# Performance work log

Hardware: AMD Instinct MI355X
Metric: run time of the kernel (lower is better)

Reference implementation:

```python
import jax, jax.numpy as jnp
import numpy as np

N_SRC0, N_DST0, N_DST1 = 100000, 20000, 4000
E0, E1 = 640000, 128000
IN_F, HID_F, OUT_F = 512, 512, 256


def _graph_conv(x_src, src, dst, W, b, n_src, n_dst):
    """DGL GraphConv, norm='both': D_out^{-1/2} A D_in^{-1/2} X W + b."""
    ones_e = jnp.ones(src.shape[0], x_src.dtype)
    out_deg = jnp.maximum(jax.ops.segment_sum(ones_e, src, num_segments=n_src), 1.0)
    in_deg = jnp.maximum(jax.ops.segment_sum(ones_e, dst, num_segments=n_dst), 1.0)
    h = x_src * (out_deg ** -0.5)[:, None]          # [n_src, F] pre-normalize
    agg = jax.ops.segment_sum(h[src], dst, num_segments=n_dst)  # gather -> scatter-add
    agg = agg * (in_deg ** -0.5)[:, None]           # [n_dst, F]
    return agg @ W + b


def setup_inputs() -> dict:
    key = jax.random.key(0)
    ks = jax.random.split(key, 8)
    x = jax.random.normal(ks[0], (N_SRC0, IN_F), jnp.float32)
    src0 = jax.random.randint(ks[1], (E0,), 0, N_SRC0)
    dst0 = jax.random.randint(ks[2], (E0,), 0, N_DST0)
    src1 = jax.random.randint(ks[3], (E1,), 0, N_DST0)
    dst1 = jax.random.randint(ks[4], (E1,), 0, N_DST1)
    W1 = jax.random.normal(ks[5], (IN_F, HID_F), jnp.float32) * (IN_F ** -0.5)
    b1 = jnp.zeros((HID_F,), jnp.float32)
    W2 = jax.random.normal(ks[6], (HID_F, OUT_F), jnp.float32) * (HID_F ** -0.5)
    b2 = jnp.zeros((OUT_F,), jnp.float32)
    return {"x": x, "src0": src0, "dst0": dst0, "src1": src1, "dst1": dst1,
            "W1": W1, "b1": b1, "W2": W2, "b2": b2,
            "n_src0": N_SRC0, "n_dst0": N_DST0, "n_dst1": N_DST1}


def reference(x, src0, dst0, src1, dst1, W1, b1, W2, b2, n_src0, n_dst0, n_dst1):
    h = jax.nn.relu(_graph_conv(x, src0, dst0, W1, b1, n_src0, n_dst0))
    out = jax.nn.relu(_graph_conv(h, src1, dst1, W2, b2, n_dst0, n_dst1))
    return out
```

## Files before the change

### kernel.cpp

```cpp
#include <hip/hip_runtime.h>

typedef unsigned short ushort_t;
typedef unsigned int uint_t;
typedef __attribute__((ext_vector_type(8))) short s8v;
typedef __attribute__((ext_vector_type(4))) float f4v;

#define NS0 100000
#define ND0 20000
#define ND1 4000
#define E0  640000
#define E1  128000
#define F   512
#define OF  256

__device__ __forceinline__ ushort_t f2b(float f) {
    uint_t u = __float_as_uint(f);
    uint_t r = (u + 0x7fffu + ((u >> 16) & 1u)) >> 16;
    return (ushort_t)r;
}
__device__ __forceinline__ float b2f_lo(uint_t u) { return __uint_as_float(u << 16); }
__device__ __forceinline__ float b2f_hi(uint_t u) { return __uint_as_float(u & 0xffff0000u); }

__global__ __launch_bounds__(256) void count_deg(const int* __restrict__ src0, const int* __restrict__ dst0,
                                                 const int* __restrict__ src1, const int* __restrict__ dst1,
                                                 int* __restrict__ cnt) {
    int i = blockIdx.x * 256 + threadIdx.x;
    int stride = gridDim.x * 256;
    for (int e = i; e < E0; e += stride) {
        atomicAdd(&cnt[src0[e]], 1);
        atomicAdd(&cnt[NS0 + dst0[e]], 1);
    }
    for (int e = i; e < E1; e += stride) {
        atomicAdd(&cnt[NS0 + ND0 + src1[e]], 1);
        atomicAdd(&cnt[NS0 + ND0 + ND0 + dst1[e]], 1);
    }
}

__global__ __launch_bounds__(1024) void pre2(const int* __restrict__ cnt, float* __restrict__ rsq, int ncnt,
                                             int* __restrict__ off0, int* __restrict__ cur0,
                                             int* __restrict__ off1, int* __restrict__ cur1) {
    if (blockIdx.x >= 2) {
        int i = (blockIdx.x - 2) * 1024 + threadIdx.x;
        if (i < ncnt) rsq[i] = rsqrtf(fmaxf((float)cnt[i], 1.0f));
        return;
    }
    const int* c = blockIdx.x ? (cnt + NS0 + ND0 + ND0) : (cnt + NS0);
    int n = blockIdx.x ? ND1 : ND0;
    int* off = blockIdx.x ? off1 : off0;
    int* cur = blockIdx.x ? cur1 : cur0;
    __shared__ int wsum[16];
    __shared__ int wexc[16];
    int lid = threadIdx.x, lane = lid & 63, w = lid >> 6;
    int ch = (n + 1023) >> 10;
    int s0 = lid * ch;
    int e0 = min(s0 + ch, n);
    int sum = 0;
    for (int i = s0; i < e0; ++i) sum += c[i];
    int s = sum;
    #pragma unroll
    for (int d = 1; d < 64; d <<= 1) { int t = __shfl_up(s, d, 64); if (lane >= d) s += t; }
    if (lane == 63) wsum[w] = s;
    __syncthreads();
    if (w == 0 && lane < 16) {
        int ws = wsum[lane];
        int ss = ws;
        #pragma unroll
        for (int d = 1; d < 16; d <<= 1) { int t = __shfl_up(ss, d, 64); if (lane >= d) ss += t; }
        wexc[lane] = ss - ws;
    }
    __syncthreads();
    int run = wexc[w] + s - sum;
    for (int i = s0; i < e0; ++i) {
        int v = c[i];
        off[i] = run; cur[i] = run;
        run += v;
    }
}

#define FBLK (E0 / 256)
#define WBLK ((F * F + F * OF) / 256)
#define XBLK (NS0 * 128 / 256)
__global__ __launch_bounds__(256) void mid_fused(const int* __restrict__ src0, const int* __restrict__ dst0,
                                                 const int* __restrict__ src1, const int* __restrict__ dst1,
                                                 int* __restrict__ cur0, int* __restrict__ cur1,
                                                 int* __restrict__ es0, int* __restrict__ es1,
                                                 const float* __restrict__ W1, const float* __restrict__ W2,
                                                 ushort_t* __restrict__ wt1, ushort_t* __restrict__ wt2,
                                                 const float* __restrict__ x, const float* __restrict__ rsq_out0,
                                                 ushort_t* __restrict__ xb) {
    if (blockIdx.x < FBLK) {
        int i = blockIdx.x * 256 + threadIdx.x;
        {
            int d = dst0[i];
            int p = atomicAdd(&cur0[d], 1);
            es0[p] = src0[i];
        }
        if (i < E1) {
            int d = dst1[i];
            int p = atomicAdd(&cur1[d], 1);
            es1[p] = src1[i];
        }
        return;
    }
    if (blockIdx.x < FBLK + WBLK) {
        int i = (blockIdx.x - FBLK) * 256 + threadIdx.x;
        if (i < F * F) {
            int k = i >> 9, n = i & (F - 1);
            wt1[n * F + k] = f2b(W1[i]);
        } else {
            int j = i - F * F;
            int k = j >> 8, n = j & (OF - 1);
            wt2[n * F + k] = f2b(W2[j]);
        }
        return;
    }
    int i = (blockIdx.x - FBLK - WBLK) * 256 + threadIdx.x;
    if (i >= NS0 * 128) return;
    int row = i >> 7;
    f4v v = __builtin_nontemporal_load(((const f4v*)x) + i);
    float sc = rsq_out0[row];
    uint2 o;
    o.x = (uint_t)f2b(v.x * sc) | ((uint_t)f2b(v.y * sc) << 16);
    o.y = (uint_t)f2b(v.z * sc) | ((uint_t)f2b(v.w * sc) << 16);
    ((uint2*)xb)[i] = o;
}

__device__ __forceinline__ void add8(float* acc, uint4 u) {
    acc[0] += b2f_lo(u.x); acc[1] += b2f_hi(u.x);
    acc[2] += b2f_lo(u.y); acc[3] += b2f_hi(u.y);
    acc[4] += b2f_lo(u.z); acc[5] += b2f_hi(u.z);
    acc[6] += b2f_lo(u.w); acc[7] += b2f_hi(u.w);
}

__global__ __launch_bounds__(256) void agg_bf16(const ushort_t* __restrict__ X, const int* __restrict__ es,
                                                const int* __restrict__ off, const int* __restrict__ cnt,
                                                const float* __restrict__ rsq_in, ushort_t* __restrict__ out,
                                                int ndst) {
    int d = __builtin_amdgcn_readfirstlane(blockIdx.x * 4 + (threadIdx.x >> 6));
    if (d >= ndst) return;
    int lane = threadIdx.x & 63;
    int base = off[d], n = cnt[d];
    const uint4* Xv = (const uint4*)X;
    float acc[8] = {0.f, 0.f, 0.f, 0.f, 0.f, 0.f, 0.f, 0.f};
    int i = 0;
    for (; i + 16 <= n; i += 16) {
        uint4 u[16];
        #pragma unroll
        for (int j = 0; j < 16; ++j) u[j] = Xv[(size_t)es[base + i + j] * 64 + lane];
        #pragma unroll
        for (int j = 0; j < 16; ++j) add8(acc, u[j]);
    }
    for (; i + 4 <= n; i += 4) {
        uint4 u[4];
        #pragma unroll
        for (int j = 0; j < 4; ++j) u[j] = Xv[(size_t)es[base + i + j] * 64 + lane];
        #pragma unroll
        for (int j = 0; j < 4; ++j) add8(acc, u[j]);
    }
    for (; i < n; ++i) add8(acc, Xv[(size_t)es[base + i] * 64 + lane]);
    float sc = rsq_in[d];
    uint4 o;
    o.x = (uint_t)f2b(acc[0] * sc) | ((uint_t)f2b(acc[1] * sc) << 16);
    o.y = (uint_t)f2b(acc[2] * sc) | ((uint_t)f2b(acc[3] * sc) << 16);
    o.z = (uint_t)f2b(acc[4] * sc) | ((uint_t)f2b(acc[5] * sc) << 16);
    o.w = (uint_t)f2b(acc[6] * sc) | ((uint_t)f2b(acc[7] * sc) << 16);
    ((uint4*)out)[(size_t)d * 64 + lane] = o;
}

template <typename OutT>
__global__ __launch_bounds__(256) void gemm128(const ushort_t* __restrict__ A, const ushort_t* __restrict__ BT,
                                               const float* __restrict__ bias, const float* __restrict__ rowScale,
                                               OutT* __restrict__ C, int M, int N, int K) {
    __shared__ __align__(16) ushort_t As[128 * 64];
    __shared__ __align__(16) ushort_t Bs[128 * 64];
    int tid = threadIdx.x;
    int lane = tid & 63, w = tid >> 6;
    int m16 = lane & 15, quad = lane >> 4;
    int wm = w & 1, wn = w >> 1;
    int bm = blockIdx.x * 128, bn = blockIdx.y * 128;
    f4v acc[4][4] = {};
    for (int k0 = 0; k0 < K; k0 += 64) {
        #pragma unroll
        for (int i = 0; i < 4; ++i) {
            int c = i * 256 + tid;
            int row = c >> 3, seg = (c & 7) * 8;
            int ra = bm + row; if (ra >= M) ra = M - 1;
            __builtin_amdgcn_global_load_lds(
                (const __attribute__((address_space(1))) uint_t*)(A + (size_t)ra * K + k0 + seg),
                (__attribute__((address_space(3))) uint_t*)(As + (size_t)c * 8), 16, 0, 0);
        }
        #pragma unroll
        for (int i = 0; i < 4; ++i) {
            int c = i * 256 + tid;
            int row = c >> 3, seg = (c & 7) * 8;
            int rb = bn + row;
            __builtin_amdgcn_global_load_lds(
                (const __attribute__((address_space(1))) uint_t*)(BT + (size_t)rb * K + k0 + seg),
                (__attribute__((address_space(3))) uint_t*)(Bs + (size_t)c * 8), 16, 0, 0);
        }
        __syncthreads();
        #pragma unroll
        for (int kc = 0; kc < 2; ++kc) {
            int co = kc * 32 + quad * 8;
            s8v af[4], bf[4];
            #pragma unroll
            for (int m = 0; m < 4; ++m)
                af[m] = *(const s8v*)&As[(wm * 64 + m * 16 + m16) * 64 + co];
            #pragma unroll
            for (int nn = 0; nn < 4; ++nn)
                bf[nn] = *(const s8v*)&Bs[(wn * 64 + nn * 16 + m16) * 64 + co];
            #pragma unroll
            for (int m = 0; m < 4; ++m)
                #pragma unroll
                for (int nn = 0; nn < 4; ++nn)
                    acc[m][nn] = __builtin_amdgcn_mfma_f32_16x16x32_bf16(af[m], bf[nn], acc[m][nn], 0, 0, 0);
        }
        __syncthreads();
    }
    #pragma unroll
    for (int m = 0; m < 4; ++m) {
        #pragma unroll
        for (int rr = 0; rr < 4; ++rr) {
            int row = bm + wm * 64 + m * 16 + quad * 4 + rr;
            if (row < M) {
                float rs = rowScale ? rowScale[row] : 1.0f;
                #pragma unroll
                for (int nn = 0; nn < 4; ++nn) {
                    int col = bn + wn * 64 + nn * 16 + m16;
                    float v = fmaxf(acc[m][nn][rr] + bias[col], 0.0f) * rs;
                    if (sizeof(OutT) == 2)
                        ((ushort_t*)C)[(size_t)row * N + col] = f2b(v);
                    else
                        ((float*)C)[(size_t)row * N + col] = v;
                }
            }
        }
    }
}

extern "C" void kernel_launch(void* const* d_in, const int* in_sizes, int n_in,
                              void* d_out, int out_size, void* d_ws, size_t ws_size,
                              hipStream_t stream) {
    (void)in_sizes; (void)n_in; (void)out_size; (void)ws_size;
    const float* x    = (const float*)d_in[0];
    const int*   src0 = (const int*)d_in[1];
    const int*   dst0 = (const int*)d_in[2];
    const int*   src1 = (const int*)d_in[3];
    const int*   dst1 = (const int*)d_in[4];
    const float* W1   = (const float*)d_in[5];
    const float* b1   = (const float*)d_in[6];
    const float* W2   = (const float*)d_in[7];
    const float* b2   = (const float*)d_in[8];
    float* out = (float*)d_out;

    char* p = (char*)d_ws;
    auto alloc = [&](size_t bytes) { char* q = p; p += (bytes + 255) & ~(size_t)255; return q; };
    const int NCNT = NS0 + ND0 + ND0 + ND1;
    int*      cnt  = (int*)alloc((size_t)NCNT * 4);
    float*    rsq  = (float*)alloc((size_t)NCNT * 4);
    int*      off0 = (int*)alloc((size_t)ND0 * 4);
    int*      cur0 = (int*)alloc((size_t)ND0 * 4);
    int*      off1 = (int*)alloc((size_t)ND1 * 4);
    int*      cur1 = (int*)alloc((size_t)ND1 * 4);
    int*      es0  = (int*)alloc((size_t)E0 * 4);
    int*      es1  = (int*)alloc((size_t)E1 * 4);
    ushort_t* wt1  = (ushort_t*)alloc((size_t)F * F * 2);
    ushort_t* wt2  = (ushort_t*)alloc((size_t)OF * F * 2);
    ushort_t* agg0 = (ushort_t*)alloc((size_t)ND0 * F * 2);
    ushort_t* h    = (ushort_t*)alloc((size_t)ND0 * F * 2);
    ushort_t* agg1 = (ushort_t*)alloc((size_t)ND1 * F * 2);
    ushort_t* xb   = (ushort_t*)alloc((size_t)NS0 * F * 2);

    const float* rsq_out0 = rsq;
    const float* rsq_in0  = rsq + NS0;
    const float* rsq_out1 = rsq + NS0 + ND0;
    const float* rsq_in1  = rsq + NS0 + ND0 + ND0;

    (void)hipMemsetAsync(cnt, 0, (size_t)NCNT * 4, stream);
    count_deg<<<E0 / 256, 256, 0, stream>>>(src0, dst0, src1, dst1, cnt);
    pre2<<<2 + (NCNT + 1023) / 1024, 1024, 0, stream>>>(cnt, rsq, NCNT, off0, cur0, off1, cur1);
    mid_fused<<<FBLK + WBLK + XBLK, 256, 0, stream>>>(src0, dst0, src1, dst1, cur0, cur1, es0, es1,
                                                      W1, W2, wt1, wt2, x, rsq_out0, xb);
    agg_bf16<<<(ND0 + 3) / 4, 256, 0, stream>>>(xb, es0, off0, cnt + NS0, rsq_in0, agg0, ND0);

    gemm128<ushort_t><<<dim3((ND0 + 127) / 128, F / 128), 256, 0, stream>>>(
        agg0, wt1, b1, rsq_out1, h, ND0, F, F);

    agg_bf16<<<(ND1 + 3) / 4, 256, 0, stream>>>(h, es1, off1, cnt + NS0 + ND0 + ND0, rsq_in1, agg1, ND1);

    gemm128<float><<<dim3((ND1 + 127) / 128, OF / 128), 256, 0, stream>>>(
        agg1, wt2, b2, nullptr, out, ND1, OF, F);
}
```

Baseline: 593.4 us.

## Merge preprocessing kernels into one cooperative kernel with grid syncs

Replaces the three preprocessing kernels (degree count, prefix scan plus rsqrt, CSR fill plus weight and x conversion) with one cooperative kernel of 1024 blocks that uses grid.sync between phases. The aim is to remove kernel launch gaps and tail effects between the small dependent stages. In exchange, the scan now runs on 256-thread blocks instead of 1024-thread ones, so each thread handles a longer serial chunk while the rest of the grid waits at the barrier. The large x conversion also moves to a grid-stride loop over fewer threads.

```diff
diff --git a/kernel.cpp b/kernel.cpp
--- a/kernel.cpp
+++ b/kernel.cpp
@@ -1,4 +1,7 @@
 #include <hip/hip_runtime.h>
+#include <hip/hip_cooperative_groups.h>
+
+namespace cg = cooperative_groups;
 
 typedef unsigned short ushort_t;
 typedef unsigned int uint_t;
@@ -12,6 +15,7 @@
 #define E1  128000
 #define F   512
 #define OF  256
+#define NCNT (NS0 + ND0 + ND0 + ND1)
 
 __device__ __forceinline__ ushort_t f2b(float f) {
     uint_t u = __float_as_uint(f);
@@ -21,108 +25,96 @@
 __device__ __forceinline__ float b2f_lo(uint_t u) { return __uint_as_float(u << 16); }
 __device__ __forceinline__ float b2f_hi(uint_t u) { return __uint_as_float(u & 0xffff0000u); }
 
-__global__ __launch_bounds__(256) void count_deg(const int* __restrict__ src0, const int* __restrict__ dst0,
-                                                 const int* __restrict__ src1, const int* __restrict__ dst1,
-                                                 int* __restrict__ cnt) {
-    int i = blockIdx.x * 256 + threadIdx.x;
-    int stride = gridDim.x * 256;
-    for (int e = i; e < E0; e += stride) {
+__global__ __launch_bounds__(256) void prep(const float* __restrict__ x,
+                                            const int* __restrict__ src0, const int* __restrict__ dst0,
+                                            const int* __restrict__ src1, const int* __restrict__ dst1,
+                                            const float* __restrict__ W1, const float* __restrict__ W2,
+                                            int* __restrict__ cnt, float* __restrict__ rsq,
+                                            int* __restrict__ off0, int* __restrict__ cur0,
+                                            int* __restrict__ off1, int* __restrict__ cur1,
+                                            int* __restrict__ es0, int* __restrict__ es1,
+                                            ushort_t* __restrict__ wt1, ushort_t* __restrict__ wt2,
+                                            ushort_t* __restrict__ xb) {
+    cg::grid_group grid = cg::this_grid();
+    const int T = gridDim.x * 256;
+    int tid = blockIdx.x * 256 + threadIdx.x;
+
+    for (int e = tid; e < E0; e += T) {
         atomicAdd(&cnt[src0[e]], 1);
         atomicAdd(&cnt[NS0 + dst0[e]], 1);
     }
-    for (int e = i; e < E1; e += stride) {
+    for (int e = tid; e < E1; e += T) {
         atomicAdd(&cnt[NS0 + ND0 + src1[e]], 1);
         atomicAdd(&cnt[NS0 + ND0 + ND0 + dst1[e]], 1);
     }
-}
-
-__global__ __launch_bounds__(1024) void pre2(const int* __restrict__ cnt, float* __restrict__ rsq, int ncnt,
-                                             int* __restrict__ off0, int* __restrict__ cur0,
-                                             int* __restrict__ off1, int* __restrict__ cur1) {
-    if (blockIdx.x >= 2) {
-        int i = (blockIdx.x - 2) * 1024 + threadIdx.x;
-        if (i < ncnt) rsq[i] = rsqrtf(fmaxf((float)cnt[i], 1.0f));
-        return;
-    }
-    const int* c = blockIdx.x ? (cnt + NS0 + ND0 + ND0) : (cnt + NS0);
-    int n = blockIdx.x ? ND1 : ND0;
-    int* off = blockIdx.x ? off1 : off0;
-    int* cur = blockIdx.x ? cur1 : cur0;
-    __shared__ int wsum[16];
-    __shared__ int wexc[16];
-    int lid = threadIdx.x, lane = lid & 63, w = lid >> 6;
-    int ch = (n + 1023) >> 10;
-    int s0 = lid * ch;
-    int e0 = min(s0 + ch, n);
-    int sum = 0;
-    for (int i = s0; i < e0; ++i) sum += c[i];
-    int s = sum;
-    #pragma unroll
-    for (int d = 1; d < 64; d <<= 1) { int t = __shfl_up(s, d, 64); if (lane >= d) s += t; }
-    if (lane == 63) wsum[w] = s;
-    __syncthreads();
-    if (w == 0 && lane < 16) {
-        int ws = wsum[lane];
-        int ss = ws;
-        #pragma unroll
-        for (int d = 1; d < 16; d <<= 1) { int t = __shfl_up(ss, d, 64); if (lane >= d) ss += t; }
-        wexc[lane] = ss - ws;
-    }
-    __syncthreads();
-    int run = wexc[w] + s - sum;
-    for (int i = s0; i < e0; ++i) {
-        int v = c[i];
-        off[i] = run; cur[i] = run;
-        run += v;
-    }
-}
-
-#define FBLK (E0 / 256)
-#define WBLK ((F * F + F * OF) / 256)
-#define XBLK (NS0 * 128 / 256)
-__global__ __launch_bounds__(256) void mid_fused(const int* __restrict__ src0, const int* __restrict__ dst0,
-                                                 const int* __restrict__ src1, const int* __restrict__ dst1,
-                                                 int* __restrict__ cur0, int* __restrict__ cur1,
-                                                 int* __restrict__ es0, int* __restrict__ es1,
-                                                 const float* __restrict__ W1, const float* __restrict__ W2,
-                                                 ushort_t* __restrict__ wt1, ushort_t* __restrict__ wt2,
-                                                 const float* __restrict__ x, const float* __restrict__ rsq_out0,
-                                                 ushort_t* __restrict__ xb) {
-    if (blockIdx.x < FBLK) {
-        int i = blockIdx.x * 256 + threadIdx.x;
-        {
-            int d = dst0[i];
-            int p = atomicAdd(&cur0[d], 1);
-            es0[p] = src0[i];
-        }
-        if (i < E1) {
-            int d = dst1[i];
-            int p = atomicAdd(&cur1[d], 1);
-            es1[p] = src1[i];
-        }
-        return;
-    }
-    if (blockIdx.x < FBLK + WBLK) {
-        int i = (blockIdx.x - FBLK) * 256 + threadIdx.x;
-        if (i < F * F) {
-            int k = i >> 9, n = i & (F - 1);
-            wt1[n * F + k] = f2b(W1[i]);
-        } else {
-            int j = i - F * F;
-            int k = j >> 8, n = j & (OF - 1);
-            wt2[n * F + k] = f2b(W2[j]);
-        }
-        return;
-    }
-    int i = (blockIdx.x - FBLK - WBLK) * 256 + threadIdx.x;
-    if (i >= NS0 * 128) return;
-    int row = i >> 7;
-    f4v v = __builtin_nontemporal_load(((const f4v*)x) + i);
-    float sc = rsq_out0[row];
-    uint2 o;
-    o.x = (uint_t)f2b(v.x * sc) | ((uint_t)f2b(v.y * sc) << 16);
-    o.y = (uint_t)f2b(v.z * sc) | ((uint_t)f2b(v.w * sc) << 16);
-    ((uint2*)xb)[i] = o;
+    for (int i = tid; i < F * F; i += T) {
+        int k = i >> 9, n = i & (F - 1);
+        wt1[n * F + k] = f2b(W1[i]);
+    }
+    for (int i = tid; i < F * OF; i += T) {
+        int k = i >> 8, n = i & (OF - 1);
+        wt2[n * F + k] = f2b(W2[i]);
+    }
+    grid.sync();
+
+    if (blockIdx.x < 2) {
+        const int* c = blockIdx.x ? (cnt + NS0 + ND0 + ND0) : (cnt + NS0);
+        int n = blockIdx.x ? ND1 : ND0;
+        int* off = blockIdx.x ? off1 : off0;
+        int* cur = blockIdx.x ? cur1 : cur0;
+        __shared__ int wsum[4];
+        __shared__ int wexc[4];
+        int lid = threadIdx.x, lane = lid & 63, w = lid >> 6;
+        int ch = (n + 255) >> 8;
+        int s0 = lid * ch;
+        int e0 = min(s0 + ch, n);
+        int sum = 0;
+        for (int i = s0; i < e0; ++i) sum += c[i];
+        int s = sum;
+        #pragma unroll
+        for (int d = 1; d < 64; d <<= 1) { int t = __shfl_up(s, d, 64); if (lane >= d) s += t; }
+        if (lane == 63) wsum[w] = s;
+        __syncthreads();
+        if (w == 0 && lane < 4) {
+            int ws = wsum[lane];
+            int ss = ws;
+            #pragma unroll
+            for (int d = 1; d < 4; d <<= 1) { int t = __shfl_up(ss, d, 64); if (lane >= d) ss += t; }
+            wexc[lane] = ss - ws;
+        }
+        __syncthreads();
+        int run = wexc[w] + s - sum;
+        for (int i = s0; i < e0; ++i) {
+            int v = c[i];
+            off[i] = run; cur[i] = run;
+            run += v;
+        }
+    } else {
+        int stride = (gridDim.x - 2) * 256;
+        for (int i = (blockIdx.x - 2) * 256 + threadIdx.x; i < NCNT; i += stride)
+            rsq[i] = rsqrtf(fmaxf((float)cnt[i], 1.0f));
+    }
+    grid.sync();
+
+    for (int e = tid; e < E0; e += T) {
+        int d = dst0[e];
+        int p = atomicAdd(&cur0[d], 1);
+        es0[p] = src0[e];
+    }
+    for (int e = tid; e < E1; e += T) {
+        int d = dst1[e];
+        int p = atomicAdd(&cur1[d], 1);
+        es1[p] = src1[e];
+    }
+    for (int q = tid; q < NS0 * 128; q += T) {
+        int row = q >> 7;
+        f4v v = __builtin_nontemporal_load(((const f4v*)x) + q);
+        float sc = rsq[row];
+        uint2 o;
+        o.x = (uint_t)f2b(v.x * sc) | ((uint_t)f2b(v.y * sc) << 16);
+        o.y = (uint_t)f2b(v.z * sc) | ((uint_t)f2b(v.w * sc) << 16);
+        ((uint2*)xb)[q] = o;
+    }
 }
 
 __device__ __forceinline__ void add8(float* acc, uint4 u) {
@@ -255,7 +247,6 @@
 
     char* p = (char*)d_ws;
     auto alloc = [&](size_t bytes) { char* q = p; p += (bytes + 255) & ~(size_t)255; return q; };
-    const int NCNT = NS0 + ND0 + ND0 + ND1;
     int*      cnt  = (int*)alloc((size_t)NCNT * 4);
     float*    rsq  = (float*)alloc((size_t)NCNT * 4);
     int*      off0 = (int*)alloc((size_t)ND0 * 4);
@@ -271,16 +262,18 @@
     ushort_t* agg1 = (ushort_t*)alloc((size_t)ND1 * F * 2);
     ushort_t* xb   = (ushort_t*)alloc((size_t)NS0 * F * 2);
 
-    const float* rsq_out0 = rsq;
     const float* rsq_in0  = rsq + NS0;
     const float* rsq_out1 = rsq + NS0 + ND0;
     const float* rsq_in1  = rsq + NS0 + ND0 + ND0;
 
     (void)hipMemsetAsync(cnt, 0, (size_t)NCNT * 4, stream);
-    count_deg<<<E0 / 256, 256, 0, stream>>>(src0, dst0, src1, dst1, cnt);
-    pre2<<<2 + (NCNT + 1023) / 1024, 1024, 0, stream>>>(cnt, rsq, NCNT, off0, cur0, off1, cur1);
-    mid_fused<<<FBLK + WBLK + XBLK, 256, 0, stream>>>(src0, dst0, src1, dst1, cur0, cur1, es0, es1,
-                                                      W1, W2, wt1, wt2, x, rsq_out0, xb);
+
+    void* args[] = {(void*)&x, (void*)&src0, (void*)&dst0, (void*)&src1, (void*)&dst1,
+                    (void*)&W1, (void*)&W2, (void*)&cnt, (void*)&rsq,
+                    (void*)&off0, (void*)&cur0, (void*)&off1, (void*)&cur1,
+                    (void*)&es0, (void*)&es1, (void*)&wt1, (void*)&wt2, (void*)&xb};
+    (void)hipLaunchCooperativeKernel((const void*)prep, dim3(1024), dim3(256), args, 0, stream);
+
     agg_bf16<<<(ND0 + 3) / 4, 256, 0, stream>>>(xb, es0, off0, cnt + NS0, rsq_in0, agg0, ND0);
 
     gemm128<ushort_t><<<dim3((ND0 + 127) / 128, F / 128), 256, 0, stream>>>(
```

Result: slower. 825.9 us (+39.2%).
